# Kernel tuning notes

Hardware: AMD Instinct MI355X
Metric: run time of the kernel (lower is better)

## Reference

```python
import jax, jax.numpy as jnp
import numpy as np

B_SZ, L_SEQ, D_MODEL, D_STATE = 4, 2048, 1024, 16


def setup_inputs() -> dict:
    key = jax.random.key(0)
    ks = jax.random.split(key, 6)
    x = jax.random.normal(ks[0], (B_SZ, L_SEQ, D_MODEL), jnp.float32)
    # HiPPO-inspired init: A_log = log(arange(1..n)).clamp(min=-7), broadcast over channels
    A_log = jnp.clip(jnp.log(jnp.arange(1, D_STATE + 1, dtype=jnp.float32)), -7.0, None)
    A_log = jnp.broadcast_to(A_log[None, :], (D_MODEL, D_STATE)).astype(jnp.float32)
    B_param = 0.02 * jax.random.normal(ks[1], (D_MODEL, D_STATE), jnp.float32)
    C_param = 0.02 * jax.random.normal(ks[2], (D_MODEL, D_STATE), jnp.float32)
    log_dt = 0.01 * jax.random.normal(ks[3], (D_MODEL,), jnp.float32) - 4.0
    in_w = jax.random.normal(ks[4], (2 * D_MODEL, D_MODEL), jnp.float32) / np.sqrt(D_MODEL).astype(np.float32)
    in_b = jnp.zeros((2 * D_MODEL,), jnp.float32)
    out_w = jax.random.normal(ks[5], (D_MODEL, D_MODEL), jnp.float32) / np.sqrt(D_MODEL).astype(np.float32)
    out_b = jnp.zeros((D_MODEL,), jnp.float32)
    ln_g = jnp.ones((D_MODEL,), jnp.float32)
    ln_b = jnp.zeros((D_MODEL,), jnp.float32)
    return {"x": x, "A_log": A_log, "B_param": B_param, "C_param": C_param,
            "log_dt": log_dt, "in_w": in_w, "in_b": in_b, "out_w": out_w,
            "out_b": out_b, "ln_g": ln_g, "ln_b": ln_b}


def _ssm_scan(u, A_log, B_param, C_param, log_dt):
    # u: (B, L, D). Builds kernel h[t,d] = sum_n A_bar[d,n]^t * C[d,n]*B[d,n]*dt[d]
    # and applies a causal depthwise convolution (via FFT; same math as conv1d).
    L = u.shape[1]
    dt = jnp.clip(jnp.exp(log_dt), 1e-4, 1.0)                      # (D,)
    A_bar = jnp.exp(-jnp.exp(A_log) * dt[:, None])                 # ZOH discretisation (D,N)
    A_bar = jnp.clip(A_bar, 1e-8, 1.0 - 1e-8)
    log_A = jnp.log(A_bar)                                         # (D,N)
    t_idx = jnp.arange(L, dtype=jnp.float32)                       # (L,)
    A_powers = jnp.exp(t_idx[:, None, None] * log_A[None, :, :])   # (L,D,N)
    cb_dt = C_param * B_param * dt[:, None]                        # (D,N)
    kernel = jnp.einsum('ldn,dn->ld', A_powers, cb_dt)             # (L,D)
    # causal conv: y[b,t,d] = sum_{tau<=t} kernel[tau,d] * u[b,t-tau,d]
    n_fft = 2 * L
    Kf = jnp.fft.rfft(kernel, n=n_fft, axis=0)                     # (n_fft/2+1, D)
    Uf = jnp.fft.rfft(u, n=n_fft, axis=1)                          # (B, n_fft/2+1, D)
    y = jnp.fft.irfft(Uf * Kf[None], n=n_fft, axis=1)[:, :L]       # (B,L,D)
    return y.astype(u.dtype)


def reference(x, A_log, B_param, C_param, log_dt, in_w, in_b, out_w, out_b, ln_g, ln_b):
    x = x.astype(jnp.float32)
    residual = x
    # LayerNorm (eps=1e-5)
    mu = jnp.mean(x, axis=-1, keepdims=True)
    var = jnp.mean(jnp.square(x - mu), axis=-1, keepdims=True)
    xn = (x - mu) * jax.lax.rsqrt(var + 1e-5) * ln_g + ln_b
    xz = xn @ in_w.T + in_b                                        # (B,L,2D)
    x_proj, z = xz[..., :D_MODEL], xz[..., D_MODEL:]
    z = jax.nn.silu(z)
    y = _ssm_scan(x_proj, A_log, B_param, C_param, log_dt)
    y = y * z
    y = y @ out_w.T + out_b
    # dropout is identity in eval mode
    return jnp.clip(y + residual, -10.0, 10.0)
```

## Files before the change

kernel.cpp:

```cpp
#include <hip/hip_runtime.h>
#include <hip/hip_bf16.h>

#define D_MODEL 1024
#define D_STATE 16
#define L_SEQ 2048
#define B_SZ 4
#define M_ROWS (B_SZ * L_SEQ)
#define N_CHUNK 32
#define C_LEN 64

typedef __attribute__((ext_vector_type(8))) short short8;
typedef __attribute__((ext_vector_type(4))) float f32x4;

#define SBAR()  asm volatile("s_barrier" ::: "memory")
#define GATE(N) asm volatile("s_waitcnt vmcnt(" #N ") lgkmcnt(0)\n\ts_barrier" ::: "memory")

typedef const unsigned short __attribute__((address_space(1))) gas_us;
typedef unsigned short __attribute__((address_space(3))) las_us;
static __device__ __forceinline__ void gload16(const unsigned short* g, unsigned short* l) {
    __builtin_amdgcn_global_load_lds((gas_us*)g, (las_us*)l, 16, 0, 0);
}

static __device__ __forceinline__ unsigned short f2bf(float f) {
    unsigned int u = __float_as_uint(f);
    unsigned int r = (u + 0x7FFFu + ((u >> 16) & 1u)) >> 16;
    return (unsigned short)r;
}
static __device__ __forceinline__ float bf2f(unsigned short u) {
    return __uint_as_float(((unsigned int)u) << 16);
}

__global__ void conv_bf16_kernel(const float* __restrict__ src,
                                 unsigned short* __restrict__ dst, int n4) {
    int i = blockIdx.x * blockDim.x + threadIdx.x;
    if (i < n4) {
        float4 v = ((const float4*)src)[i];
        ushort4 o;
        o.x = f2bf(v.x); o.y = f2bf(v.y); o.z = f2bf(v.z); o.w = f2bf(v.w);
        ((ushort4*)dst)[i] = o;
    }
}

__global__ __launch_bounds__(256) void ln_kernel(const float* __restrict__ x,
                                                 const float* __restrict__ g,
                                                 const float* __restrict__ b,
                                                 unsigned short* __restrict__ xn) {
    int row = blockIdx.x;
    int t = threadIdx.x;
    const float4* xr = (const float4*)(x + (size_t)row * D_MODEL);
    float4 v = xr[t];
    float s  = v.x + v.y + v.z + v.w;
    float ss = v.x * v.x + v.y * v.y + v.z * v.z + v.w * v.w;
    #pragma unroll
    for (int o = 32; o > 0; o >>= 1) {
        s  += __shfl_down(s,  o);
        ss += __shfl_down(ss, o);
    }
    __shared__ float sbuf[8];
    int wid = t >> 6;
    if ((t & 63) == 0) { sbuf[wid] = s; sbuf[4 + wid] = ss; }
    __syncthreads();
    float S  = sbuf[0] + sbuf[1] + sbuf[2] + sbuf[3];
    float SS = sbuf[4] + sbuf[5] + sbuf[6] + sbuf[7];
    float mu  = S * (1.0f / D_MODEL);
    float var = SS * (1.0f / D_MODEL) - mu * mu;
    float inv = rsqrtf(var + 1e-5f);
    float4 gv = ((const float4*)g)[t];
    float4 bv = ((const float4*)b)[t];
    ushort4 o;
    o.x = f2bf((v.x - mu) * inv * gv.x + bv.x);
    o.y = f2bf((v.y - mu) * inv * gv.y + bv.y);
    o.z = f2bf((v.z - mu) * inv * gv.z + bv.z);
    o.w = f2bf((v.w - mu) * inv * gv.w + bv.w);
    ((ushort4*)(xn + (size_t)row * D_MODEL))[t] = o;
}

#define MFMA16(ACC, I0, AV, BV) { \
    _Pragma("unroll") for (int i_ = 0; i_ < 4; ++i_) { \
        _Pragma("unroll") for (int jf_ = 0; jf_ < 4; ++jf_) \
            ACC[(I0) + i_][jf_] = __builtin_amdgcn_mfma_f32_16x16x32_bf16( \
                AV[i_], BV[jf_], ACC[(I0) + i_][jf_], 0, 0, 0); } }

#define STAGE1A(J) { size_t ko_ = (size_t)(J) * 32; int so_ = ((J) & 3) * 16384; \
    gload16(pA0 + ko_, dA0 + so_); gload16(pA1 + ko_, dA1 + so_); }
#define STAGE1B(J) { size_t ko_ = (size_t)(J) * 32; int so_ = ((J) & 3) * 16384; \
    gload16(pB0 + ko_, dB0 + so_); gload16(pB1 + ko_, dB1 + so_); }

#define G1_TILE(J, DOSTAGE, TRAIL) { \
    const int slot_ = (J) & 3; \
    const char* rA_ = ldsA_rd + slot_ * 32768; \
    const char* rB_ = ldsB_rd + slot_ * 32768; \
    short8 av[4], bv[4]; \
    _Pragma("unroll") for (int j_ = 0; j_ < 4; ++j_) bv[j_] = *(const short8*)(rB_ + j_ * 1024); \
    _Pragma("unroll") for (int i_ = 0; i_ < 4; ++i_) av[i_] = *(const short8*)(rA_ + i_ * 1024); \
    if (DOSTAGE) { STAGE1A((J) + 3); } \
    SBAR(); \
    __builtin_amdgcn_s_setprio(1); \
    MFMA16(acc, 0, av, bv); \
    __builtin_amdgcn_s_setprio(0); \
    SBAR(); \
    _Pragma("unroll") for (int i_ = 0; i_ < 4; ++i_) av[i_] = *(const short8*)(rA_ + 4096 + i_ * 1024); \
    if (DOSTAGE) { STAGE1B((J) + 3); } \
    SBAR(); \
    __builtin_amdgcn_s_setprio(1); \
    MFMA16(acc, 4, av, bv); \
    __builtin_amdgcn_s_setprio(0); \
    TRAIL; \
}

__global__ __launch_bounds__(512, 2) void gemm1_kernel(const unsigned short* __restrict__ A,
                                                       const unsigned short* __restrict__ Bt,
                                                       const float* __restrict__ bias,
                                                       unsigned short* __restrict__ u_bf,
                                                       unsigned short* __restrict__ zs) {
    __shared__ __align__(16) unsigned short lds[4][2][8192];
    const int K = D_MODEL;

    int t = threadIdx.x;
    int lane = t & 63;
    int wave = t >> 6;
    int wm = wave >> 2;
    int wn = wave & 3;

    int bid = blockIdx.x;
    int swz = (bid & 7) * 32 + (bid >> 3);
    int m0 = (swz >> 3) * 256;
    int n0 = (swz & 7) * 256;

    int srow = lane >> 2;
    int sk = ((lane & 3) * 8) ^ ((lane & 32) >> 1);
    const unsigned short* pA0 = A  + (size_t)(m0 + wave * 16 + srow) * K + sk;
    const unsigned short* pA1 = pA0 + (size_t)128 * K;
    const unsigned short* pB0 = Bt + (size_t)(n0 + wave * 16 + srow) * K + sk;
    const unsigned short* pB1 = pB0 + (size_t)128 * K;

    unsigned short* dA0 = &lds[0][0][wave * 512];
    unsigned short* dA1 = &lds[0][0][(8 + wave) * 512];
    unsigned short* dB0 = &lds[0][1][wave * 512];
    unsigned short* dB1 = &lds[0][1][(8 + wave) * 512];

    int off_base = (lane & 15) * 64 + (((lane >> 4) * 16) ^ ((lane & 8) * 4));
    const char* ldsA_rd = (const char*)(&lds[0][0][0]) + wm * 8192 + off_base;
    const char* ldsB_rd = (const char*)(&lds[0][1][0]) + wn * 4096 + off_base;

    f32x4 acc[8][4] = {};

    STAGE1A(0); STAGE1B(0); STAGE1A(1); STAGE1B(1); STAGE1A(2); STAGE1B(2);
    GATE(8);

    #pragma unroll 1
    for (int j = 0; j < 29; ++j) { G1_TILE(j, true, GATE(8)); }
    G1_TILE(29, false, GATE(4));
    G1_TILE(30, false, GATE(0));
    G1_TILE(31, false, (void)0);

    int col = lane & 15;
    int quad = lane >> 4;
    #pragma unroll
    for (int jf = 0; jf < 4; ++jf) {
        int n = n0 + wn * 64 + jf * 16 + col;
        float bs = bias[n];
        bool isU = (n < D_MODEL);
        #pragma unroll
        for (int i = 0; i < 8; ++i) {
            #pragma unroll
            for (int r = 0; r < 4; ++r) {
                int m = m0 + wm * 128 + i * 16 + quad * 4 + r;
                float v = acc[i][jf][r] + bs;
                if (isU) {
                    u_bf[(size_t)m * D_MODEL + n] = f2bf(v);
                } else {
                    float sv = v / (1.0f + __expf(-v));
                    zs[(size_t)m * D_MODEL + (n - D_MODEL)] = f2bf(sv);
                }
            }
        }
    }
}

#define STAGE2(J) { size_t ko_ = (size_t)(J) * 32; int so_ = ((J) & 3) * 12288; \
    gload16(pA0 + ko_, dA + so_); gload16(pB0 + ko_, dB0 + so_); gload16(pB1 + ko_, dB1 + so_); }

#define G2_TILE(J, DOSTAGE, TRAIL) { \
    const int slot_ = (J) & 3; \
    const char* rA_ = ldsA_rd + slot_ * 24576; \
    const char* rB_ = ldsB_rd + slot_ * 24576; \
    short8 av[4], bv[4]; \
    _Pragma("unroll") for (int i_ = 0; i_ < 4; ++i_) av[i_] = *(const short8*)(rA_ + i_ * 1024); \
    _Pragma("unroll") for (int j_ = 0; j_ < 4; ++j_) bv[j_] = *(const short8*)(rB_ + j_ * 1024); \
    if (DOSTAGE) { STAGE2((J) + 3); } \
    SBAR(); \
    __builtin_amdgcn_s_setprio(1); \
    MFMA16(acc, 0, av, bv); \
    __builtin_amdgcn_s_setprio(0); \
    TRAIL; \
}

__global__ __launch_bounds__(512, 2) void gemm2_kernel(const unsigned short* __restrict__ A,
                                                       const unsigned short* __restrict__ Bt,
                                                       const float* __restrict__ bias,
                                                       float* __restrict__ out_f,
                                                       const float* __restrict__ resid) {
    __shared__ __align__(16) unsigned short lds[4][12288];
    const int K = D_MODEL;

    int t = threadIdx.x;
    int lane = t & 63;
    int wave = t >> 6;
    int wm = wave >> 2;
    int wn = wave & 3;

    int bid = blockIdx.x;
    int swz = (bid & 7) * 32 + (bid >> 3);
    int m0 = (swz >> 2) * 128;
    int n0 = (swz & 3) * 256;

    int srow = lane >> 2;
    int sk = ((lane & 3) * 8) ^ ((lane & 32) >> 1);
    const unsigned short* pA0 = A  + (size_t)(m0 + wave * 16 + srow) * K + sk;
    const unsigned short* pB0 = Bt + (size_t)(n0 + wave * 16 + srow) * K + sk;
    const unsigned short* pB1 = pB0 + (size_t)128 * K;

    unsigned short* dA  = &lds[0][wave * 512];
    unsigned short* dB0 = &lds[0][4096 + wave * 512];
    unsigned short* dB1 = &lds[0][8192 + wave * 512];

    int off_base = (lane & 15) * 64 + (((lane >> 4) * 16) ^ ((lane & 8) * 4));
    const char* ldsA_rd = (const char*)(&lds[0][0]) + wm * 4096 + off_base;
    const char* ldsB_rd = (const char*)(&lds[0][0]) + 8192 + wn * 4096 + off_base;

    f32x4 acc[4][4] = {};

    STAGE2(0); STAGE2(1); STAGE2(2);
    GATE(6);

    #pragma unroll 1
    for (int j = 0; j < 29; ++j) { G2_TILE(j, true, GATE(6)); }
    G2_TILE(29, false, GATE(3));
    G2_TILE(30, false, GATE(0));
    G2_TILE(31, false, (void)0);

    int col = lane & 15;
    int quad = lane >> 4;
    #pragma unroll
    for (int jf = 0; jf < 4; ++jf) {
        int n = n0 + wn * 64 + jf * 16 + col;
        float bs = bias[n];
        #pragma unroll
        for (int i = 0; i < 4; ++i) {
            #pragma unroll
            for (int r = 0; r < 4; ++r) {
                int m = m0 + wm * 64 + i * 16 + quad * 4 + r;
                float y = acc[i][jf][r] + bs + resid[(size_t)m * D_MODEL + n];
                y = fminf(10.0f, fmaxf(-10.0f, y));
                out_f[(size_t)m * D_MODEL + n] = y;
            }
        }
    }
}

static __device__ __forceinline__ void load_params(const float* __restrict__ A_log,
                                                   const float* __restrict__ log_dt,
                                                   int d, float* ab, float& dt_out) {
    float dt = fminf(1.0f, fmaxf(1e-4f, __expf(log_dt[d])));
    #pragma unroll
    for (int n = 0; n < D_STATE; n++) {
        float a = __expf(-__expf(A_log[d * D_STATE + n]) * dt);
        ab[n] = fminf(1.0f - 1e-8f, fmaxf(1e-8f, a));
    }
    dt_out = dt;
}

__global__ __launch_bounds__(256) void scan1_kernel(const unsigned short* __restrict__ u,
                                                    const float* __restrict__ A_log,
                                                    const float* __restrict__ log_dt,
                                                    float* __restrict__ s_local) {
    int gid = blockIdx.x * 256 + threadIdx.x;
    int d = gid & (D_MODEL - 1);
    int c = (gid >> 10) & (N_CHUNK - 1);
    int b = gid >> 15;

    float ab[D_STATE], dt;
    load_params(A_log, log_dt, d, ab, dt);

    float s[D_STATE];
    #pragma unroll
    for (int n = 0; n < D_STATE; n++) s[n] = 0.0f;

    const unsigned short* up = u + ((size_t)(b * L_SEQ + c * C_LEN)) * D_MODEL + d;
    for (int t = 0; t < C_LEN; t++) {
        float uv = bf2f(up[(size_t)t * D_MODEL]);
        #pragma unroll
        for (int n = 0; n < D_STATE; n++) s[n] = fmaf(ab[n], s[n], uv);
    }
    float* sl = s_local + ((size_t)(b * N_CHUNK + c) * D_STATE) * D_MODEL + d;
    #pragma unroll
    for (int n = 0; n < D_STATE; n++) sl[(size_t)n * D_MODEL] = s[n];
}

__global__ __launch_bounds__(256) void scan_combine_kernel(const float* __restrict__ s_local,
                                                           const float* __restrict__ A_log,
                                                           const float* __restrict__ log_dt,
                                                           float* __restrict__ s_init) {
    int gid = blockIdx.x * 256 + threadIdx.x;
    int d = gid & (D_MODEL - 1);
    int n = (gid >> 10) & (D_STATE - 1);
    int b = gid >> 14;

    float dt = fminf(1.0f, fmaxf(1e-4f, __expf(log_dt[d])));
    float a = __expf(-__expf(A_log[d * D_STATE + n]) * dt);
    a = fminf(1.0f - 1e-8f, fmaxf(1e-8f, a));
    float aP = a;
    #pragma unroll
    for (int q = 0; q < 6; q++) aP = aP * aP;

    float s = 0.0f;
    size_t stride_c = (size_t)D_STATE * D_MODEL;
    const float* sl = s_local + ((size_t)b * N_CHUNK * D_STATE + n) * D_MODEL + d;
    float* si = s_init + ((size_t)b * N_CHUNK * D_STATE + n) * D_MODEL + d;
    si[0] = 0.0f;
    for (int c = 1; c < N_CHUNK; c++) {
        s = fmaf(aP, s, sl[(size_t)(c - 1) * stride_c]);
        si[(size_t)c * stride_c] = s;
    }
}

__global__ __launch_bounds__(256) void scan2_kernel(const unsigned short* __restrict__ u,
                                                    const unsigned short* __restrict__ zs,
                                                    const float* __restrict__ A_log,
                                                    const float* __restrict__ Bp,
                                                    const float* __restrict__ Cp,
                                                    const float* __restrict__ log_dt,
                                                    const float* __restrict__ s_init,
                                                    unsigned short* __restrict__ yz) {
    int gid = blockIdx.x * 256 + threadIdx.x;
    int d = gid & (D_MODEL - 1);
    int c = (gid >> 10) & (N_CHUNK - 1);
    int b = gid >> 15;

    float ab[D_STATE], dt;
    load_params(A_log, log_dt, d, ab, dt);
    float cb[D_STATE];
    #pragma unroll
    for (int n = 0; n < D_STATE; n++)
        cb[n] = Cp[d * D_STATE + n] * Bp[d * D_STATE + n] * dt;

    float s[D_STATE];
    const float* si = s_init + ((size_t)(b * N_CHUNK + c) * D_STATE) * D_MODEL + d;
    #pragma unroll
    for (int n = 0; n < D_STATE; n++) s[n] = si[(size_t)n * D_MODEL];

    size_t m0 = (size_t)(b * L_SEQ + c * C_LEN);
    const unsigned short* up = u + m0 * D_MODEL + d;
    const unsigned short* zp = zs + m0 * D_MODEL + d;
    unsigned short* yp = yz + m0 * D_MODEL + d;

    for (int t = 0; t < C_LEN; t++) {
        float uv = bf2f(up[(size_t)t * D_MODEL]);
        #pragma unroll
        for (int n = 0; n < D_STATE; n++) s[n] = fmaf(ab[n], s[n], uv);
        float y = 0.0f;
        #pragma unroll
        for (int n = 0; n < D_STATE; n++) y = fmaf(cb[n], s[n], y);
        float zv = bf2f(zp[(size_t)t * D_MODEL]);
        yp[(size_t)t * D_MODEL] = f2bf(y * zv);
    }
}

extern "C" void kernel_launch(void* const* d_in, const int* in_sizes, int n_in,
                              void* d_out, int out_size, void* d_ws, size_t ws_size,
                              hipStream_t stream) {
    const float* x       = (const float*)d_in[0];
    const float* A_log   = (const float*)d_in[1];
    const float* B_param = (const float*)d_in[2];
    const float* C_param = (const float*)d_in[3];
    const float* log_dt  = (const float*)d_in[4];
    const float* in_w    = (const float*)d_in[5];
    const float* in_b    = (const float*)d_in[6];
    const float* out_w   = (const float*)d_in[7];
    const float* out_b   = (const float*)d_in[8];
    const float* ln_g    = (const float*)d_in[9];
    const float* ln_b    = (const float*)d_in[10];
    float* out = (float*)d_out;

    char* ws = (char*)d_ws;
    size_t off = 0;
    unsigned short* xn = (unsigned short*)(ws + off); off += (size_t)M_ROWS * D_MODEL * 2;
    unsigned short* w1 = (unsigned short*)(ws + off); off += (size_t)2 * D_MODEL * D_MODEL * 2;
    unsigned short* u  = (unsigned short*)(ws + off); off += (size_t)M_ROWS * D_MODEL * 2;
    unsigned short* zs = (unsigned short*)(ws + off); off += (size_t)M_ROWS * D_MODEL * 2;
    unsigned short* yz = (unsigned short*)(ws + off); off += (size_t)M_ROWS * D_MODEL * 2;
    unsigned short* w2 = (unsigned short*)(ws + off); off += (size_t)D_MODEL * D_MODEL * 2;
    float* s_local = (float*)(ws + off); off += (size_t)B_SZ * N_CHUNK * D_STATE * D_MODEL * 4;
    float* s_init  = (float*)(ws + off); off += (size_t)B_SZ * N_CHUNK * D_STATE * D_MODEL * 4;

    {
        int n4 = 2 * D_MODEL * D_MODEL / 4;
        conv_bf16_kernel<<<(n4 + 255) / 256, 256, 0, stream>>>(in_w, w1, n4);
    }
    {
        int n4 = D_MODEL * D_MODEL / 4;
        conv_bf16_kernel<<<(n4 + 255) / 256, 256, 0, stream>>>(out_w, w2, n4);
    }

    ln_kernel<<<M_ROWS, 256, 0, stream>>>(x, ln_g, ln_b, xn);

    gemm1_kernel<<<256, 512, 0, stream>>>(xn, w1, in_b, u, zs);

    scan1_kernel<<<(B_SZ * N_CHUNK * D_MODEL) / 256, 256, 0, stream>>>(u, A_log, log_dt, s_local);
    scan_combine_kernel<<<(B_SZ * D_STATE * D_MODEL) / 256, 256, 0, stream>>>(s_local, A_log, log_dt, s_init);
    scan2_kernel<<<(B_SZ * N_CHUNK * D_MODEL) / 256, 256, 0, stream>>>(
        u, zs, A_log, B_param, C_param, log_dt, s_init, yz);

    gemm2_kernel<<<256, 512, 0, stream>>>(yz, w2, out_b, out, x);
}
```

Baseline: 214.3 us.

## Merge LN and weight conversion kernels; retile gemm1 to 128x256 with 512 blocks

Fuses the LayerNorm and two weight bf16-conversion kernels into one prep kernel, dropping two launches. gemm1 moves from 256x256 tiles on 256 blocks to the 128x256 tiling already used by gemm2, so it runs 512 blocks and gets better CU occupancy and load balance. The two GEMMs now share one macro for the main loop. Epilogues are reordered so each row writes its four column fragments together and the silu/u branch is chosen once per block. Smaller tiles lower A/B reuse per block and add global traffic.

```diff
diff --git a/kernel.cpp b/kernel.cpp
--- a/kernel.cpp
+++ b/kernel.cpp
@@ -30,170 +30,144 @@
     return __uint_as_float(((unsigned int)u) << 16);
 }
 
-__global__ void conv_bf16_kernel(const float* __restrict__ src,
-                                 unsigned short* __restrict__ dst, int n4) {
-    int i = blockIdx.x * blockDim.x + threadIdx.x;
-    if (i < n4) {
-        float4 v = ((const float4*)src)[i];
+__global__ __launch_bounds__(256) void prep_kernel(const float* __restrict__ x,
+                                                   const float* __restrict__ g,
+                                                   const float* __restrict__ b,
+                                                   unsigned short* __restrict__ xn,
+                                                   const float* __restrict__ in_w,
+                                                   unsigned short* __restrict__ w1,
+                                                   const float* __restrict__ out_w,
+                                                   unsigned short* __restrict__ w2) {
+    __shared__ float sbuf[8];
+    int bid = blockIdx.x;
+    int t = threadIdx.x;
+    if (bid < M_ROWS) {
+        int row = bid;
+        const float4* xr = (const float4*)(x + (size_t)row * D_MODEL);
+        float4 v = xr[t];
+        float s  = v.x + v.y + v.z + v.w;
+        float ss = v.x * v.x + v.y * v.y + v.z * v.z + v.w * v.w;
+        #pragma unroll
+        for (int o = 32; o > 0; o >>= 1) {
+            s  += __shfl_down(s,  o);
+            ss += __shfl_down(ss, o);
+        }
+        int wid = t >> 6;
+        if ((t & 63) == 0) { sbuf[wid] = s; sbuf[4 + wid] = ss; }
+        __syncthreads();
+        float S  = sbuf[0] + sbuf[1] + sbuf[2] + sbuf[3];
+        float SS = sbuf[4] + sbuf[5] + sbuf[6] + sbuf[7];
+        float mu  = S * (1.0f / D_MODEL);
+        float var = SS * (1.0f / D_MODEL) - mu * mu;
+        float inv = rsqrtf(var + 1e-5f);
+        float4 gv = ((const float4*)g)[t];
+        float4 bv = ((const float4*)b)[t];
+        ushort4 o;
+        o.x = f2bf((v.x - mu) * inv * gv.x + bv.x);
+        o.y = f2bf((v.y - mu) * inv * gv.y + bv.y);
+        o.z = f2bf((v.z - mu) * inv * gv.z + bv.z);
+        o.w = f2bf((v.w - mu) * inv * gv.w + bv.w);
+        ((ushort4*)(xn + (size_t)row * D_MODEL))[t] = o;
+    } else if (bid < M_ROWS + 2048) {
+        int i = (bid - M_ROWS) * 256 + t;
+        float4 v = ((const float4*)in_w)[i];
         ushort4 o;
         o.x = f2bf(v.x); o.y = f2bf(v.y); o.z = f2bf(v.z); o.w = f2bf(v.w);
-        ((ushort4*)dst)[i] = o;
-    }
-}
-
-__global__ __launch_bounds__(256) void ln_kernel(const float* __restrict__ x,
-                                                 const float* __restrict__ g,
-                                                 const float* __restrict__ b,
-                                                 unsigned short* __restrict__ xn) {
-    int row = blockIdx.x;
-    int t = threadIdx.x;
-    const float4* xr = (const float4*)(x + (size_t)row * D_MODEL);
-    float4 v = xr[t];
-    float s  = v.x + v.y + v.z + v.w;
-    float ss = v.x * v.x + v.y * v.y + v.z * v.z + v.w * v.w;
-    #pragma unroll
-    for (int o = 32; o > 0; o >>= 1) {
-        s  += __shfl_down(s,  o);
-        ss += __shfl_down(ss, o);
-    }
-    __shared__ float sbuf[8];
-    int wid = t >> 6;
-    if ((t & 63) == 0) { sbuf[wid] = s; sbuf[4 + wid] = ss; }
-    __syncthreads();
-    float S  = sbuf[0] + sbuf[1] + sbuf[2] + sbuf[3];
-    float SS = sbuf[4] + sbuf[5] + sbuf[6] + sbuf[7];
-    float mu  = S * (1.0f / D_MODEL);
-    float var = SS * (1.0f / D_MODEL) - mu * mu;
-    float inv = rsqrtf(var + 1e-5f);
-    float4 gv = ((const float4*)g)[t];
-    float4 bv = ((const float4*)b)[t];
-    ushort4 o;
-    o.x = f2bf((v.x - mu) * inv * gv.x + bv.x);
-    o.y = f2bf((v.y - mu) * inv * gv.y + bv.y);
-    o.z = f2bf((v.z - mu) * inv * gv.z + bv.z);
-    o.w = f2bf((v.w - mu) * inv * gv.w + bv.w);
-    ((ushort4*)(xn + (size_t)row * D_MODEL))[t] = o;
-}
-
-#define MFMA16(ACC, I0, AV, BV) { \
+        ((ushort4*)w1)[i] = o;
+    } else {
+        int i = (bid - M_ROWS - 2048) * 256 + t;
+        float4 v = ((const float4*)out_w)[i];
+        ushort4 o;
+        o.x = f2bf(v.x); o.y = f2bf(v.y); o.z = f2bf(v.z); o.w = f2bf(v.w);
+        ((ushort4*)w2)[i] = o;
+    }
+}
+
+#define MFMA16(ACC, AV, BV) { \
     _Pragma("unroll") for (int i_ = 0; i_ < 4; ++i_) { \
         _Pragma("unroll") for (int jf_ = 0; jf_ < 4; ++jf_) \
-            ACC[(I0) + i_][jf_] = __builtin_amdgcn_mfma_f32_16x16x32_bf16( \
-                AV[i_], BV[jf_], ACC[(I0) + i_][jf_], 0, 0, 0); } }
-
-#define STAGE1A(J) { size_t ko_ = (size_t)(J) * 32; int so_ = ((J) & 3) * 16384; \
-    gload16(pA0 + ko_, dA0 + so_); gload16(pA1 + ko_, dA1 + so_); }
-#define STAGE1B(J) { size_t ko_ = (size_t)(J) * 32; int so_ = ((J) & 3) * 16384; \
-    gload16(pB0 + ko_, dB0 + so_); gload16(pB1 + ko_, dB1 + so_); }
-
-#define G1_TILE(J, DOSTAGE, TRAIL) { \
-    const int slot_ = (J) & 3; \
-    const char* rA_ = ldsA_rd + slot_ * 32768; \
-    const char* rB_ = ldsB_rd + slot_ * 32768; \
-    short8 av[4], bv[4]; \
-    _Pragma("unroll") for (int j_ = 0; j_ < 4; ++j_) bv[j_] = *(const short8*)(rB_ + j_ * 1024); \
-    _Pragma("unroll") for (int i_ = 0; i_ < 4; ++i_) av[i_] = *(const short8*)(rA_ + i_ * 1024); \
-    if (DOSTAGE) { STAGE1A((J) + 3); } \
-    SBAR(); \
-    __builtin_amdgcn_s_setprio(1); \
-    MFMA16(acc, 0, av, bv); \
-    __builtin_amdgcn_s_setprio(0); \
-    SBAR(); \
-    _Pragma("unroll") for (int i_ = 0; i_ < 4; ++i_) av[i_] = *(const short8*)(rA_ + 4096 + i_ * 1024); \
-    if (DOSTAGE) { STAGE1B((J) + 3); } \
-    SBAR(); \
-    __builtin_amdgcn_s_setprio(1); \
-    MFMA16(acc, 4, av, bv); \
-    __builtin_amdgcn_s_setprio(0); \
-    TRAIL; \
-}
-
-__global__ __launch_bounds__(512, 2) void gemm1_kernel(const unsigned short* __restrict__ A,
-                                                       const unsigned short* __restrict__ Bt,
-                                                       const float* __restrict__ bias,
-                                                       unsigned short* __restrict__ u_bf,
-                                                       unsigned short* __restrict__ zs) {
-    __shared__ __align__(16) unsigned short lds[4][2][8192];
-    const int K = D_MODEL;
-
-    int t = threadIdx.x;
-    int lane = t & 63;
-    int wave = t >> 6;
-    int wm = wave >> 2;
-    int wn = wave & 3;
-
-    int bid = blockIdx.x;
-    int swz = (bid & 7) * 32 + (bid >> 3);
-    int m0 = (swz >> 3) * 256;
-    int n0 = (swz & 7) * 256;
-
-    int srow = lane >> 2;
-    int sk = ((lane & 3) * 8) ^ ((lane & 32) >> 1);
-    const unsigned short* pA0 = A  + (size_t)(m0 + wave * 16 + srow) * K + sk;
-    const unsigned short* pA1 = pA0 + (size_t)128 * K;
-    const unsigned short* pB0 = Bt + (size_t)(n0 + wave * 16 + srow) * K + sk;
-    const unsigned short* pB1 = pB0 + (size_t)128 * K;
-
-    unsigned short* dA0 = &lds[0][0][wave * 512];
-    unsigned short* dA1 = &lds[0][0][(8 + wave) * 512];
-    unsigned short* dB0 = &lds[0][1][wave * 512];
-    unsigned short* dB1 = &lds[0][1][(8 + wave) * 512];
-
-    int off_base = (lane & 15) * 64 + (((lane >> 4) * 16) ^ ((lane & 8) * 4));
-    const char* ldsA_rd = (const char*)(&lds[0][0][0]) + wm * 8192 + off_base;
-    const char* ldsB_rd = (const char*)(&lds[0][1][0]) + wn * 4096 + off_base;
-
-    f32x4 acc[8][4] = {};
-
-    STAGE1A(0); STAGE1B(0); STAGE1A(1); STAGE1B(1); STAGE1A(2); STAGE1B(2);
-    GATE(8);
-
-    #pragma unroll 1
-    for (int j = 0; j < 29; ++j) { G1_TILE(j, true, GATE(8)); }
-    G1_TILE(29, false, GATE(4));
-    G1_TILE(30, false, GATE(0));
-    G1_TILE(31, false, (void)0);
-
-    int col = lane & 15;
-    int quad = lane >> 4;
-    #pragma unroll
-    for (int jf = 0; jf < 4; ++jf) {
-        int n = n0 + wn * 64 + jf * 16 + col;
-        float bs = bias[n];
-        bool isU = (n < D_MODEL);
-        #pragma unroll
-        for (int i = 0; i < 8; ++i) {
-            #pragma unroll
-            for (int r = 0; r < 4; ++r) {
-                int m = m0 + wm * 128 + i * 16 + quad * 4 + r;
-                float v = acc[i][jf][r] + bs;
-                if (isU) {
-                    u_bf[(size_t)m * D_MODEL + n] = f2bf(v);
-                } else {
-                    float sv = v / (1.0f + __expf(-v));
-                    zs[(size_t)m * D_MODEL + (n - D_MODEL)] = f2bf(sv);
-                }
-            }
-        }
-    }
-}
-
-#define STAGE2(J) { size_t ko_ = (size_t)(J) * 32; int so_ = ((J) & 3) * 12288; \
+            ACC[i_][jf_] = __builtin_amdgcn_mfma_f32_16x16x32_bf16( \
+                AV[i_], BV[jf_], ACC[i_][jf_], 0, 0, 0); } }
+
+#define STAGE(J) { size_t ko_ = (size_t)(J) * 32; int so_ = ((J) & 3) * 12288; \
     gload16(pA0 + ko_, dA + so_); gload16(pB0 + ko_, dB0 + so_); gload16(pB1 + ko_, dB1 + so_); }
 
-#define G2_TILE(J, DOSTAGE, TRAIL) { \
+#define G_TILE(J, DOSTAGE, TRAIL) { \
     const int slot_ = (J) & 3; \
     const char* rA_ = ldsA_rd + slot_ * 24576; \
     const char* rB_ = ldsB_rd + slot_ * 24576; \
     short8 av[4], bv[4]; \
     _Pragma("unroll") for (int i_ = 0; i_ < 4; ++i_) av[i_] = *(const short8*)(rA_ + i_ * 1024); \
     _Pragma("unroll") for (int j_ = 0; j_ < 4; ++j_) bv[j_] = *(const short8*)(rB_ + j_ * 1024); \
-    if (DOSTAGE) { STAGE2((J) + 3); } \
+    if (DOSTAGE) { STAGE((J) + 3); } \
     SBAR(); \
     __builtin_amdgcn_s_setprio(1); \
-    MFMA16(acc, 0, av, bv); \
+    MFMA16(acc, av, bv); \
     __builtin_amdgcn_s_setprio(0); \
     TRAIL; \
+}
+
+#define GEMM_PREAMBLE(APTR, BPTR, NWGM_SHIFT, NWGN_MASK, NBLK_PER_XCD) \
+    const int K = D_MODEL; \
+    int t = threadIdx.x; \
+    int lane = t & 63; \
+    int wave = t >> 6; \
+    int wm = wave >> 2; \
+    int wn = wave & 3; \
+    int bid = blockIdx.x; \
+    int swz = (bid & 7) * (NBLK_PER_XCD) + (bid >> 3); \
+    int m0 = (swz >> (NWGM_SHIFT)) * 128; \
+    int n0 = (swz & (NWGN_MASK)) * 256; \
+    int srow = lane >> 2; \
+    int sk = ((lane & 3) * 8) ^ ((lane & 32) >> 1); \
+    const unsigned short* pA0 = (APTR) + (size_t)(m0 + wave * 16 + srow) * K + sk; \
+    const unsigned short* pB0 = (BPTR) + (size_t)(n0 + wave * 16 + srow) * K + sk; \
+    const unsigned short* pB1 = pB0 + (size_t)128 * K; \
+    unsigned short* dA  = &lds[0][wave * 512]; \
+    unsigned short* dB0 = &lds[0][4096 + wave * 512]; \
+    unsigned short* dB1 = &lds[0][8192 + wave * 512]; \
+    int off_base = (lane & 15) * 64 + (((lane >> 4) * 16) ^ ((lane & 8) * 4)); \
+    const char* ldsA_rd = (const char*)(&lds[0][0]) + wm * 4096 + off_base; \
+    const char* ldsB_rd = (const char*)(&lds[0][0]) + 8192 + wn * 4096 + off_base; \
+    f32x4 acc[4][4] = {}; \
+    STAGE(0); STAGE(1); STAGE(2); \
+    GATE(6); \
+    _Pragma("unroll 1") \
+    for (int j = 0; j < 29; ++j) { G_TILE(j, true, GATE(6)); } \
+    G_TILE(29, false, GATE(3)); \
+    G_TILE(30, false, GATE(0)); \
+    G_TILE(31, false, (void)0);
+
+__global__ __launch_bounds__(512, 2) void gemm1_kernel(const unsigned short* __restrict__ A,
+                                                       const unsigned short* __restrict__ Bt,
+                                                       const float* __restrict__ bias,
+                                                       unsigned short* __restrict__ u_bf,
+                                                       unsigned short* __restrict__ zs) {
+    __shared__ __align__(16) unsigned short lds[4][12288];
+    GEMM_PREAMBLE(A, Bt, 3, 7, 64)
+
+    int col = lane & 15;
+    int quad = lane >> 4;
+    float bs[4];
+    #pragma unroll
+    for (int jf = 0; jf < 4; ++jf) bs[jf] = bias[n0 + wn * 64 + jf * 16 + col];
+    bool isU = (n0 < D_MODEL);
+    int nbase = isU ? (n0 + wn * 64 + col) : (n0 - D_MODEL + wn * 64 + col);
+    unsigned short* obase = isU ? u_bf : zs;
+    #pragma unroll
+    for (int i = 0; i < 4; ++i) {
+        #pragma unroll
+        for (int r = 0; r < 4; ++r) {
+            int m = m0 + wm * 64 + i * 16 + quad * 4 + r;
+            unsigned short* orow = obase + (size_t)m * D_MODEL + nbase;
+            #pragma unroll
+            for (int jf = 0; jf < 4; ++jf) {
+                float v = acc[i][jf][r] + bs[jf];
+                if (!isU) v = v / (1.0f + __expf(-v));
+                orow[jf * 16] = f2bf(v);
+            }
+        }
+    }
 }
 
 __global__ __launch_bounds__(512, 2) void gemm2_kernel(const unsigned short* __restrict__ A,
@@ -202,58 +176,25 @@
                                                        float* __restrict__ out_f,
                                                        const float* __restrict__ resid) {
     __shared__ __align__(16) unsigned short lds[4][12288];
-    const int K = D_MODEL;
-
-    int t = threadIdx.x;
-    int lane = t & 63;
-    int wave = t >> 6;
-    int wm = wave >> 2;
-    int wn = wave & 3;
-
-    int bid = blockIdx.x;
-    int swz = (bid & 7) * 32 + (bid >> 3);
-    int m0 = (swz >> 2) * 128;
-    int n0 = (swz & 3) * 256;
-
-    int srow = lane >> 2;
-    int sk = ((lane & 3) * 8) ^ ((lane & 32) >> 1);
-    const unsigned short* pA0 = A  + (size_t)(m0 + wave * 16 + srow) * K + sk;
-    const unsigned short* pB0 = Bt + (size_t)(n0 + wave * 16 + srow) * K + sk;
-    const unsigned short* pB1 = pB0 + (size_t)128 * K;
-
-    unsigned short* dA  = &lds[0][wave * 512];
-    unsigned short* dB0 = &lds[0][4096 + wave * 512];
-    unsigned short* dB1 = &lds[0][8192 + wave * 512];
-
-    int off_base = (lane & 15) * 64 + (((lane >> 4) * 16) ^ ((lane & 8) * 4));
-    const char* ldsA_rd = (const char*)(&lds[0][0]) + wm * 4096 + off_base;
-    const char* ldsB_rd = (const char*)(&lds[0][0]) + 8192 + wn * 4096 + off_base;
-
-    f32x4 acc[4][4] = {};
-
-    STAGE2(0); STAGE2(1); STAGE2(2);
-    GATE(6);
-
-    #pragma unroll 1
-    for (int j = 0; j < 29; ++j) { G2_TILE(j, true, GATE(6)); }
-    G2_TILE(29, false, GATE(3));
-    G2_TILE(30, false, GATE(0));
-    G2_TILE(31, false, (void)0);
+    GEMM_PREAMBLE(A, Bt, 2, 3, 32)
 
     int col = lane & 15;
     int quad = lane >> 4;
-    #pragma unroll
-    for (int jf = 0; jf < 4; ++jf) {
-        int n = n0 + wn * 64 + jf * 16 + col;
-        float bs = bias[n];
-        #pragma unroll
-        for (int i = 0; i < 4; ++i) {
+    float bs[4];
+    #pragma unroll
+    for (int jf = 0; jf < 4; ++jf) bs[jf] = bias[n0 + wn * 64 + jf * 16 + col];
+    #pragma unroll
+    for (int i = 0; i < 4; ++i) {
+        #pragma unroll
+        for (int r = 0; r < 4; ++r) {
+            int m = m0 + wm * 64 + i * 16 + quad * 4 + r;
+            const float* rrow = resid + (size_t)m * D_MODEL + n0 + wn * 64 + col;
+            float* orow = out_f + (size_t)m * D_MODEL + n0 + wn * 64 + col;
             #pragma unroll
-            for (int r = 0; r < 4; ++r) {
-                int m = m0 + wm * 64 + i * 16 + quad * 4 + r;
-                float y = acc[i][jf][r] + bs + resid[(size_t)m * D_MODEL + n];
+            for (int jf = 0; jf < 4; ++jf) {
+                float y = acc[i][jf][r] + bs[jf] + rrow[jf * 16];
                 y = fminf(10.0f, fmaxf(-10.0f, y));
-                out_f[(size_t)m * D_MODEL + n] = y;
+                orow[jf * 16] = y;
             }
         }
     }
@@ -394,18 +335,9 @@
     float* s_local = (float*)(ws + off); off += (size_t)B_SZ * N_CHUNK * D_STATE * D_MODEL * 4;
     float* s_init  = (float*)(ws + off); off += (size_t)B_SZ * N_CHUNK * D_STATE * D_MODEL * 4;
 
-    {
-        int n4 = 2 * D_MODEL * D_MODEL / 4;
-        conv_bf16_kernel<<<(n4 + 255) / 256, 256, 0, stream>>>(in_w, w1, n4);
-    }
-    {
-        int n4 = D_MODEL * D_MODEL / 4;
-        conv_bf16_kernel<<<(n4 + 255) / 256, 256, 0, stream>>>(out_w, w2, n4);
-    }
-
-    ln_kernel<<<M_ROWS, 256, 0, stream>>>(x, ln_g, ln_b, xn);
-
-    gemm1_kernel<<<256, 512, 0, stream>>>(xn, w1, in_b, u, zs);
+    prep_kernel<<<M_ROWS + 2048 + 1024, 256, 0, stream>>>(x, ln_g, ln_b, xn, in_w, w1, out_w, w2);
+
+    gemm1_kernel<<<512, 512, 0, stream>>>(xn, w1, in_b, u, zs);
 
     scan1_kernel<<<(B_SZ * N_CHUNK * D_MODEL) / 256, 256, 0, stream>>>(u, A_log, log_dt, s_local);
     scan_combine_kernel<<<(B_SZ * D_STATE * D_MODEL) / 256, 256, 0, stream>>>(s_local, A_log, log_dt, s_init);
```

Result: faster. 210.1 us (-2.0%).
